# Kernel optimization log

Hardware: AMD Instinct MI355X
Metric: run time of the kernel (lower is better)

The kernel has to match this reference:

```python
import jax, jax.numpy as jnp
import numpy as np

N_IN, N_OUT, K, G = 128, 128, 3, 8
BATCH = 512
GRID_MIN, GRID_MAX = -1.0, 1.0
EDGES = N_IN * N_OUT


def setup_inputs() -> dict:
    key = jax.random.key(0)
    k1, k2 = jax.random.split(key)
    # inputs inside the grid range so splines are active
    x = jax.random.uniform(k1, (BATCH, N_IN), dtype=jnp.float32,
                           minval=GRID_MIN, maxval=GRID_MAX)
    # per-edge extended uniform knot vector: G+2K+1 points (k extra on each side)
    h = (GRID_MAX - GRID_MIN) / G
    knots_1d = jnp.linspace(GRID_MIN - K * h, GRID_MAX + K * h,
                            G + 2 * K + 1, dtype=jnp.float32)
    knots = jnp.broadcast_to(knots_1d, (EDGES, G + 2 * K + 1))
    c_basis = (jax.random.normal(k2, (EDGES, G + K), dtype=jnp.float32) * 0.1)
    c_spl = jnp.ones((N_OUT, N_IN), jnp.float32)
    c_res = jnp.ones((N_OUT, N_IN), jnp.float32)
    bias = jnp.zeros((N_OUT,), jnp.float32)
    return {"x": x, "knots": knots, "c_basis": c_basis,
            "c_spl": c_spl, "c_res": c_res, "bias": bias}


def _extend(x):
    # (batch, n_in) -> (edges, batch) with edge index = o*n_in + i
    batch = x.shape[0]
    return jnp.broadcast_to(x[:, None, :], (batch, N_OUT, N_IN)).reshape(batch, EDGES).T


def _basis(x, knots):
    # Cox-de Boor recursion; returns (edges, G+K, batch)
    x_ext = _extend(x)                   # (edges, batch)
    grid = knots[:, :, None]             # (edges, G+2K+1, 1)
    x_in = x_ext[:, None, :]             # (edges, 1, batch)
    b = ((x_in >= grid[:, :-1]) & (x_in < grid[:, 1:])).astype(jnp.float32)
    for order in range(1, K + 1):
        left = (x_in - grid[:, :-(order + 1)]) / (grid[:, order:-1] - grid[:, :-(order + 1)])
        right = (grid[:, order + 1:] - x_in) / (grid[:, order + 1:] - grid[:, 1:-order])
        b = left * b[:, :-1] + right * b[:, 1:]
    return b


def reference(x, knots, c_basis, c_spl, c_res, bias):
    batch = x.shape[0]
    bi = _basis(x, knots)                           # (edges, G+K, batch)
    spl = jnp.einsum('eg,egb->eb', c_basis, bi).T   # (batch, edges)
    y = c_spl.reshape(1, EDGES) * spl
    x_ext = _extend(x).T                            # (batch, edges)
    y = y + c_res.reshape(1, EDGES) * jax.nn.silu(x_ext)
    y = jnp.sum(y.reshape(batch, N_OUT, N_IN), axis=2) + bias
    return y
```

## Files before the change

### kernel.cpp

```cpp
#include <hip/hip_runtime.h>
#include <math.h>

#define N_IN  128
#define N_OUT 128
#define BATCH 512
#define NK    11
#define TBV   16
#define TOV   16
#define STR   776

typedef float f32x4  __attribute__((ext_vector_type(4)));
typedef short bf16x8 __attribute__((ext_vector_type(8)));

__device__ __forceinline__ unsigned short f2bf(float f) {
    unsigned u = __float_as_uint(f);
    u += 0x7FFFu + ((u >> 16) & 1u);
    return (unsigned short)(u >> 16);
}

__global__ __launch_bounds__(256) void kan_kernel(
    const float* __restrict__ x,
    const float* __restrict__ cbasis,
    const float* __restrict__ cspl,
    const float* __restrict__ cres,
    const float* __restrict__ bias,
    float* __restrict__ y)
{
    __shared__ short sA[TBV * STR];
    __shared__ short sW[TOV * STR];
    __shared__ float sAcc[4 * 256];

    const int b0 = blockIdx.x * TBV;
    const int o0 = blockIdx.y * TOV;
    const int t  = threadIdx.x;
    const int w  = t >> 6;
    const int l  = t & 63;
    const int mn = l & 15;
    const int kq = (l >> 4) * 8;

    f32x4 acc = {0.f, 0.f, 0.f, 0.f};

    for (int hh = 0; hh < 2; ++hh) {
        for (int p = t; p < (TBV * STR) / 8; p += 256)
            *(int4*)&sA[p * 8] = make_int4(0, 0, 0, 0);
        __syncthreads();

        for (int p = t; p < TBV * 64; p += 256) {
            const int b  = p >> 6, il = p & 63;
            const int i  = hh * 64 + il;
            const float xv = x[(b0 + b) * N_IN + i];
            const float u  = (xv + 1.75f) * 4.0f;
            float jf = floorf(u);
            jf = fminf(fmaxf(jf, 3.0f), 10.0f);
            const float tt = u - jf;
            const float omt = 1.0f - tt;
            const float t2 = tt * tt, t3 = t2 * tt;
            const float B0 = omt * omt * omt * (1.0f / 6.0f);
            const float B1 = (3.0f * t3 - 6.0f * t2 + 4.0f) * (1.0f / 6.0f);
            const float B2 = (-3.0f * t3 + 3.0f * t2 + 3.0f * tt + 1.0f) * (1.0f / 6.0f);
            const float B3 = t3 * (1.0f / 6.0f);
            const int base = (int)jf - 3;
            const float sig = 1.0f / (1.0f + __expf(-xv));
            short* dst = &sA[b * STR + il * 12];
            dst[base]     = (short)f2bf(B0);
            dst[base + 1] = (short)f2bf(B1);
            dst[base + 2] = (short)f2bf(B2);
            dst[base + 3] = (short)f2bf(B3);
            dst[11]       = (short)f2bf(xv * sig);
        }

        for (int p = t; p < TOV * 64; p += 256) {
            const int o_l = p >> 6, il = p & 63;
            const int i   = hh * 64 + il;
            const int e   = (o0 + o_l) * N_IN + i;
            const float s = cspl[e];
            const float* src = cbasis + (size_t)e * NK;
            unsigned short hv[12];
            #pragma unroll
            for (int g = 0; g < 11; ++g) hv[g] = f2bf(s * src[g]);
            hv[11] = f2bf(cres[e]);
            unsigned d[6];
            #pragma unroll
            for (int j = 0; j < 6; ++j)
                d[j] = (unsigned)hv[2 * j] | ((unsigned)hv[2 * j + 1] << 16);
            short* dst = &sW[o_l * STR + il * 12];
            *(uint2*)(dst)     = make_uint2(d[0], d[1]);
            *(uint2*)(dst + 4) = make_uint2(d[2], d[3]);
            *(uint2*)(dst + 8) = make_uint2(d[4], d[5]);
        }
        __syncthreads();

        const short* aB = &sA[mn * STR + w * 192 + kq];
        const short* bB = &sW[mn * STR + w * 192 + kq];
        #pragma unroll
        for (int s = 0; s < 6; ++s) {
            bf16x8 af  = *(const bf16x8*)(aB + s * 32);
            bf16x8 bf_ = *(const bf16x8*)(bB + s * 32);
            acc = __builtin_amdgcn_mfma_f32_16x16x32_bf16(af, bf_, acc, 0, 0, 0);
        }
        __syncthreads();
    }

    #pragma unroll
    for (int r = 0; r < 4; ++r)
        sAcc[w * 256 + ((l >> 4) * 4 + r) * 16 + mn] = acc[r];
    __syncthreads();
    {
        const int m2 = t >> 4, n2 = t & 15;
        const float sum = sAcc[t] + sAcc[256 + t] + sAcc[512 + t] + sAcc[768 + t];
        y[(b0 + m2) * N_OUT + (o0 + n2)] = sum + bias[o0 + n2];
    }
}

extern "C" void kernel_launch(void* const* d_in, const int* in_sizes, int n_in,
                              void* d_out, int out_size, void* d_ws, size_t ws_size,
                              hipStream_t stream) {
    const float* x      = (const float*)d_in[0];
    const float* cbasis = (const float*)d_in[2];
    const float* cspl   = (const float*)d_in[3];
    const float* cres   = (const float*)d_in[4];
    const float* bias   = (const float*)d_in[5];
    float* y = (float*)d_out;

    dim3 grid(BATCH / TBV, N_OUT / TOV);
    kan_kernel<<<grid, 256, 0, stream>>>(x, cbasis, cspl, cres, bias, y);
}
```

Baseline: 71.35 us.

## Prepack bf16 weights in a separate kernel and load MFMA B fragments directly

Adds a small pre-kernel that scales c_basis by c_spl, appends c_res, and packs the result to bf16 in a workspace once per call. The main kernel then reads its weight fragments straight from global memory into registers, so it no longer converts weights per block or stages them in shared memory. The two K-halves are merged into one pass, and each basis row is written as three 64-bit words built with shifts, which removes the separate zero-fill pass and cuts barriers. The cost is an extra kernel launch plus a global round trip for the packed weights, and more registers per thread to hold twelve weight fragments.

```diff
diff --git a/kernel.cpp b/kernel.cpp
--- a/kernel.cpp
+++ b/kernel.cpp
@@ -7,10 +7,12 @@
 #define NK    11
 #define TBV   16
 #define TOV   16
-#define STR   776
+#define KTOT  1536
+#define ASTR  1544
 
 typedef float f32x4  __attribute__((ext_vector_type(4)));
 typedef short bf16x8 __attribute__((ext_vector_type(8)));
+typedef unsigned long long u64;
 
 __device__ __forceinline__ unsigned short f2bf(float f) {
     unsigned u = __float_as_uint(f);
@@ -18,16 +20,34 @@
     return (unsigned short)(u >> 16);
 }
 
+__global__ __launch_bounds__(128) void w_pack(
+    const float* __restrict__ cbasis, const float* __restrict__ cspl,
+    const float* __restrict__ cres, unsigned short* __restrict__ w2)
+{
+    const int e = blockIdx.x * 128 + threadIdx.x;
+    const float s = cspl[e];
+    const float* src = cbasis + (size_t)e * NK;
+    unsigned short h[12];
+    #pragma unroll
+    for (int g = 0; g < NK; ++g) h[g] = f2bf(s * src[g]);
+    h[11] = f2bf(cres[e]);
+    unsigned d[6];
+    #pragma unroll
+    for (int j = 0; j < 6; ++j)
+        d[j] = (unsigned)h[2 * j] | ((unsigned)h[2 * j + 1] << 16);
+    unsigned short* dst = w2 + (size_t)e * 12;
+    *(uint2*)(dst)     = make_uint2(d[0], d[1]);
+    *(uint2*)(dst + 4) = make_uint2(d[2], d[3]);
+    *(uint2*)(dst + 8) = make_uint2(d[4], d[5]);
+}
+
 __global__ __launch_bounds__(256) void kan_kernel(
     const float* __restrict__ x,
-    const float* __restrict__ cbasis,
-    const float* __restrict__ cspl,
-    const float* __restrict__ cres,
+    const unsigned short* __restrict__ w2,
     const float* __restrict__ bias,
     float* __restrict__ y)
 {
-    __shared__ short sA[TBV * STR];
-    __shared__ short sW[TOV * STR];
+    __shared__ short sA[TBV * ASTR];
     __shared__ float sAcc[4 * 256];
 
     const int b0 = blockIdx.x * TBV;
@@ -38,67 +58,54 @@
     const int mn = l & 15;
     const int kq = (l >> 4) * 8;
 
+    const unsigned short* wb = w2 + (size_t)(o0 + mn) * KTOT + w * 384 + kq;
+    bf16x8 wf[12];
+    #pragma unroll
+    for (int s = 0; s < 12; ++s)
+        wf[s] = *(const bf16x8*)(wb + s * 32);
+
+    #pragma unroll
+    for (int it = 0; it < 8; ++it) {
+        const int p = t + it * 256;
+        const int b = p >> 7, i = p & 127;
+        const float xv = x[(b0 + b) * N_IN + i];
+        const float u  = (xv + 1.75f) * 4.0f;
+        float jf = floorf(u);
+        jf = fminf(fmaxf(jf, 3.0f), 10.0f);
+        const float tt = u - jf;
+        const float omt = 1.0f - tt;
+        const float t2 = tt * tt, t3 = t2 * tt;
+        const float B0 = omt * omt * omt * (1.0f / 6.0f);
+        const float B1 = (3.0f * t3 - 6.0f * t2 + 4.0f) * (1.0f / 6.0f);
+        const float B2 = (-3.0f * t3 + 3.0f * t2 + 3.0f * tt + 1.0f) * (1.0f / 6.0f);
+        const float B3 = t3 * (1.0f / 6.0f);
+        const int base = (int)jf - 3;
+        const float sig = 1.0f / (1.0f + __expf(-xv));
+        const u64 v4 = (u64)f2bf(B0) | ((u64)f2bf(B1) << 16)
+                     | ((u64)f2bf(B2) << 32) | ((u64)f2bf(B3) << 48);
+        const int sh = base * 16;
+        u64 q0, q1, q2;
+        if (sh < 64) {
+            q0 = v4 << sh;
+            q1 = sh ? (v4 >> (64 - sh)) : 0ull;
+            q2 = 0ull;
+        } else {
+            q0 = 0ull;
+            q1 = v4 << (sh - 64);
+            q2 = (sh > 64) ? (v4 >> (128 - sh)) : 0ull;
+        }
+        q2 |= (u64)f2bf(xv * sig) << 48;
+        u64* dst = (u64*)&sA[b * ASTR + i * 12];
+        dst[0] = q0; dst[1] = q1; dst[2] = q2;
+    }
+    __syncthreads();
+
     f32x4 acc = {0.f, 0.f, 0.f, 0.f};
-
-    for (int hh = 0; hh < 2; ++hh) {
-        for (int p = t; p < (TBV * STR) / 8; p += 256)
-            *(int4*)&sA[p * 8] = make_int4(0, 0, 0, 0);
-        __syncthreads();
-
-        for (int p = t; p < TBV * 64; p += 256) {
-            const int b  = p >> 6, il = p & 63;
-            const int i  = hh * 64 + il;
-            const float xv = x[(b0 + b) * N_IN + i];
-            const float u  = (xv + 1.75f) * 4.0f;
-            float jf = floorf(u);
-            jf = fminf(fmaxf(jf, 3.0f), 10.0f);
-            const float tt = u - jf;
-            const float omt = 1.0f - tt;
-            const float t2 = tt * tt, t3 = t2 * tt;
-            const float B0 = omt * omt * omt * (1.0f / 6.0f);
-            const float B1 = (3.0f * t3 - 6.0f * t2 + 4.0f) * (1.0f / 6.0f);
-            const float B2 = (-3.0f * t3 + 3.0f * t2 + 3.0f * tt + 1.0f) * (1.0f / 6.0f);
-            const float B3 = t3 * (1.0f / 6.0f);
-            const int base = (int)jf - 3;
-            const float sig = 1.0f / (1.0f + __expf(-xv));
-            short* dst = &sA[b * STR + il * 12];
-            dst[base]     = (short)f2bf(B0);
-            dst[base + 1] = (short)f2bf(B1);
-            dst[base + 2] = (short)f2bf(B2);
-            dst[base + 3] = (short)f2bf(B3);
-            dst[11]       = (short)f2bf(xv * sig);
-        }
-
-        for (int p = t; p < TOV * 64; p += 256) {
-            const int o_l = p >> 6, il = p & 63;
-            const int i   = hh * 64 + il;
-            const int e   = (o0 + o_l) * N_IN + i;
-            const float s = cspl[e];
-            const float* src = cbasis + (size_t)e * NK;
-            unsigned short hv[12];
-            #pragma unroll
-            for (int g = 0; g < 11; ++g) hv[g] = f2bf(s * src[g]);
-            hv[11] = f2bf(cres[e]);
-            unsigned d[6];
-            #pragma unroll
-            for (int j = 0; j < 6; ++j)
-                d[j] = (unsigned)hv[2 * j] | ((unsigned)hv[2 * j + 1] << 16);
-            short* dst = &sW[o_l * STR + il * 12];
-            *(uint2*)(dst)     = make_uint2(d[0], d[1]);
-            *(uint2*)(dst + 4) = make_uint2(d[2], d[3]);
-            *(uint2*)(dst + 8) = make_uint2(d[4], d[5]);
-        }
-        __syncthreads();
-
-        const short* aB = &sA[mn * STR + w * 192 + kq];
-        const short* bB = &sW[mn * STR + w * 192 + kq];
-        #pragma unroll
-        for (int s = 0; s < 6; ++s) {
-            bf16x8 af  = *(const bf16x8*)(aB + s * 32);
-            bf16x8 bf_ = *(const bf16x8*)(bB + s * 32);
-            acc = __builtin_amdgcn_mfma_f32_16x16x32_bf16(af, bf_, acc, 0, 0, 0);
-        }
-        __syncthreads();
+    const short* aB = &sA[mn * ASTR + w * 384 + kq];
+    #pragma unroll
+    for (int s = 0; s < 12; ++s) {
+        bf16x8 af = *(const bf16x8*)(aB + s * 32);
+        acc = __builtin_amdgcn_mfma_f32_16x16x32_bf16(af, wf[s], acc, 0, 0, 0);
     }
 
     #pragma unroll
@@ -121,7 +128,9 @@
     const float* cres   = (const float*)d_in[4];
     const float* bias   = (const float*)d_in[5];
     float* y = (float*)d_out;
+    unsigned short* w2 = (unsigned short*)d_ws;
 
+    w_pack<<<128, 128, 0, stream>>>(cbasis, cspl, cres, w2);
     dim3 grid(BATCH / TBV, N_OUT / TOV);
-    kan_kernel<<<grid, 256, 0, stream>>>(x, cbasis, cspl, cres, bias, y);
+    kan_kernel<<<grid, 256, 0, stream>>>(x, w2, bias, y);
 }
```

Result: faster. 69.01 us (-3.3%).
